# Kernel tuning notes

Measured on AMD Instinct MI355X. Metric: run time of the kernel, lower is better.

Reference implementation:

```python
import jax, jax.numpy as jnp
import numpy as np

B, C, H, W = 4, 128, 128, 128
G, K = 4, 3
P = K * K
STRIDE, PAD, DIL = 1, 1, 1
OFFSET_SCALE = 1.0


def setup_inputs() -> dict:
    key = jax.random.key(0)
    k1, k2, k3, k4 = jax.random.split(key, 4)
    inp = jax.random.normal(k1, (B, C, H, W), jnp.float32)
    # offset / mask linear params (zero-init in source; small random here for a
    # nontrivial sampling pattern -- same math, different param values)
    W_off = jax.random.normal(k2, (C, G * P * 2), jnp.float32) * 0.01
    b_off = jax.random.normal(k3, (G * P * 2,), jnp.float32) * 0.5
    W_mask = jax.random.normal(k4, (C, G * P), jnp.float32) * 0.02
    b_mask = jnp.zeros((G * P,), jnp.float32)
    return {"inp": inp, "W_off": W_off, "b_off": b_off, "W_mask": W_mask, "b_mask": b_mask}


def _dcnv3_core(x, offset, mask):
    # x: (b,h,w,c)  offset: (b,h,w,G*P*2)  mask: (b,h,w,G*P)
    b, h, w, c = x.shape
    gc = c // G
    xp = jnp.pad(x, ((0, 0), (PAD, PAD), (PAD, PAD), (0, 0)))
    H_in, W_in = h + 2 * PAD, w + 2 * PAD
    H_out = (H_in - (DIL * (K - 1) + 1)) // STRIDE + 1
    W_out = (W_in - (DIL * (K - 1) + 1)) // STRIDE + 1
    Q = H_out * W_out

    # reference points, normalized to padded size (matches _get_reference_points)
    base = (DIL * (K - 1)) // 2 + 0.5
    ref_y = (base + jnp.arange(H_out, dtype=jnp.float32) * STRIDE) / H_in
    ref_x = (base + jnp.arange(W_out, dtype=jnp.float32) * STRIDE) / W_in
    ref = jnp.stack(jnp.broadcast_arrays(ref_x[None, :], ref_y[:, None]), -1)  # (Ho,Wo,2) as (x,y)

    # dilation grid (matches _generate_dilation_grids; torch meshgrid flatten is x-major)
    off0 = -((DIL * (K - 1)) // 2)
    ks = off0 + jnp.arange(K, dtype=jnp.float32) * DIL
    gx = jnp.repeat(ks, K) / W_in  # (P,)
    gy = jnp.tile(ks, K) / H_in
    grid = jnp.stack([gx, gy], -1)  # (P,2), identical for every group

    norm = jnp.array([W_in, H_in], jnp.float32)
    loc = (ref[None, :, :, None, None, :]
           + grid[None, None, None, None, :, :] * OFFSET_SCALE
           + offset.reshape(b, H_out, W_out, G, P, 2) * (OFFSET_SCALE / norm))  # (b,Ho,Wo,G,P,2)

    # grid_sample(bilinear, zeros, align_corners=False): pixel = loc*size - 0.5
    px = loc[..., 0] * W_in - 0.5
    py = loc[..., 1] * H_in - 0.5
    x0 = jnp.floor(px); y0 = jnp.floor(py)
    tx = px - x0; ty = py - y0
    x0i = x0.astype(jnp.int32); y0i = y0.astype(jnp.int32)

    xg = xp.reshape(b, H_in * W_in, G, gc)

    def corner(ix, iy, wgt):
        valid = (ix >= 0) & (ix < W_in) & (iy >= 0) & (iy < H_in)
        lin = jnp.clip(iy, 0, H_in - 1) * W_in + jnp.clip(ix, 0, W_in - 1)
        idx = lin.reshape(b, Q, G, P).transpose(0, 1, 3, 2).reshape(b, Q * P, G)
        g = jnp.take_along_axis(xg, idx[..., None], axis=1)  # (b,Q*P,G,gc)
        wv = jnp.where(valid, wgt, 0.0).reshape(b, Q, G, P).transpose(0, 1, 3, 2).reshape(b, Q * P, G, 1)
        return g * wv

    val = (corner(x0i, y0i, (1 - tx) * (1 - ty))
           + corner(x0i + 1, y0i, tx * (1 - ty))
           + corner(x0i, y0i + 1, (1 - tx) * ty)
           + corner(x0i + 1, y0i + 1, tx * ty))  # (b,Q*P,G,gc)

    m = mask.reshape(b, Q, G, P).transpose(0, 1, 3, 2).reshape(b, Q, P, G, 1)
    out = (val.reshape(b, Q, P, G, gc) * m).sum(axis=2)  # (b,Q,G,gc)
    return out.reshape(b, H_out, W_out, G * gc)


def reference(inp, W_off, b_off, W_mask, b_mask):
    b, c, h, w = inp.shape
    x = inp.reshape(b, h, w, c)  # torch .view reinterpretation (faithful to source)
    offset = x @ W_off + b_off  # (b,h,w,G*P*2)
    mask = jax.nn.softmax((x @ W_mask + b_mask).reshape(b, h, w, G, P), axis=-1).reshape(b, h, w, G * P)
    out = _dcnv3_core(x, offset, mask)  # (b,h,w,c)
    return out.reshape(b, c, h, w)
```

## Files before the change

kernel.cpp:

```cpp
#include <hip/hip_runtime.h>


#define NPIX 65536

typedef unsigned int uint;
typedef unsigned short ushort;
typedef __attribute__((ext_vector_type(8))) short short8v;
typedef __attribute__((ext_vector_type(4))) float f32x4;

__device__ __forceinline__ ushort f2bf(float f) {
  uint u = __float_as_uint(f);
  u += 0x7FFFu + ((u >> 16) & 1u);
  return (ushort)(u >> 16);
}
__device__ __forceinline__ uint pkbf(float lo, float hi) {
  return (uint)f2bf(lo) | ((uint)f2bf(hi) << 16);
}
__device__ __forceinline__ float bflo(uint d) { return __uint_as_float(d << 16); }
__device__ __forceinline__ float bfhi(uint d) { return __uint_as_float(d & 0xFFFF0000u); }
__device__ __forceinline__ ushort f2h(float f) {
  union { _Float16 h; ushort u; } cv;
  cv.h = (_Float16)f;
  return cv.u;
}
__device__ __forceinline__ float h2f_lo(uint u) {
  union { ushort s; _Float16 h; } cv;
  cv.s = (ushort)(u & 0xFFFFu);
  return (float)cv.h;
}
__device__ __forceinline__ float h2f_hi(uint u) {
  union { ushort s; _Float16 h; } cv;
  cv.s = (ushort)(u >> 16);
  return (float)cv.h;
}

union U8 { uint u[4]; short8v v; };

__device__ __forceinline__ float wcol(const float* __restrict__ Woff,
                                      const float* __restrict__ Wmask,
                                      int g, int k, int n) {
  if (n < 18) return Woff[k * 72 + g * 18 + n];
  if (n < 27) return Wmask[k * 36 + g * 9 + (n - 18)];
  return 0.f;
}

__global__ __launch_bounds__(256) void dcn_wpack(
    const float* __restrict__ Woff, const float* __restrict__ boff,
    const float* __restrict__ Wmask, const float* __restrict__ bmask,
    uint* __restrict__ wpk, float* __restrict__ wb) {
  const int idx = (blockIdx.x << 8) + threadIdx.x;
  {
    const int f = idx >> 8;
    const int widx = idx & 255;
    const int lane = widx >> 2, epair = widx & 3;
    const int kt = f & 3, nt = (f >> 2) & 1, g = f >> 3;
    const int k0 = kt * 32 + (lane >> 4) * 8 + epair * 2;
    const int n = nt * 16 + (lane & 15);
    wpk[idx] = pkbf(wcol(Woff, Wmask, g, k0, n), wcol(Woff, Wmask, g, k0 + 1, n));
  }
  if (blockIdx.x == 0 && threadIdx.x < 128) {
    const int g = threadIdx.x >> 5, n = threadIdx.x & 31;
    float bv;
    if (n < 18) bv = boff[g * 18 + n];
    else if (n < 27) bv = bmask[g * 9 + (n - 18)];
    else bv = 0.f;
    wb[threadIdx.x] = bv;
  }
}

__global__ __launch_bounds__(256) void dcn_lin2(
    const float* __restrict__ x, const uint* __restrict__ wpk,
    const float* __restrict__ wb, ushort* __restrict__ ws16,
    ushort* __restrict__ x16) {
  __shared__ __align__(16) uint lds[64 * 68];
  const int pbase = blockIdx.x << 6;
  const int t = threadIdx.x;

  {
    const int px = t >> 2, part = t & 3;
    const int pix = pbase + px;
    const float* xp = x + (size_t)pix * 128 + part * 8;
    const int bb = pix >> 14, yx = pix & 16383;
#pragma unroll
    for (int g = 0; g < 4; ++g) {
      const float4 a = *(const float4*)(xp + g * 32);
      const float4 b4 = *(const float4*)(xp + g * 32 + 4);
      uint4 s;
      s.x = pkbf(a.x, a.y);
      s.y = pkbf(a.z, a.w);
      s.z = pkbf(b4.x, b4.y);
      s.w = pkbf(b4.z, b4.w);
      *(uint4*)(lds + px * 68 + g * 16 + part * 4) = s;
      *(uint4*)(x16 + ((((size_t)((g << 2) | bb) << 14) | yx) << 5) + part * 8) = s;
    }
  }
  __syncthreads();

  const int wv = t >> 6;
  const int lane = t & 63;
  const int lrow = lane & 15;
  const int lhi = lane >> 4;
  const int pxrow = (wv << 4) + lrow;

  U8 afr[4];
#pragma unroll
  for (int kt = 0; kt < 4; ++kt) {
    const uint4 v = *(const uint4*)(lds + pxrow * 68 + kt * 16 + lhi * 4);
    afr[kt].u[0] = v.x; afr[kt].u[1] = v.y;
    afr[kt].u[2] = v.z; afr[kt].u[3] = v.w;
  }
  __syncthreads();

  f32x4 acc[4][2];
#pragma unroll
  for (int g = 0; g < 4; ++g)
#pragma unroll
    for (int nt = 0; nt < 2; ++nt) {
      const float bv = wb[(g << 5) + (nt << 4) + lrow];
      acc[g][nt] = (f32x4){bv, bv, bv, bv};
    }

#pragma unroll
  for (int kt = 0; kt < 4; ++kt)
#pragma unroll
    for (int g = 0; g < 4; ++g)
#pragma unroll
      for (int nt = 0; nt < 2; ++nt) {
        U8 bf;
        const uint4 bv =
            *(const uint4*)(wpk + ((g << 3) + (nt << 2) + kt) * 256 + (lane << 2));
        bf.u[0] = bv.x; bf.u[1] = bv.y; bf.u[2] = bv.z; bf.u[3] = bv.w;
        acc[g][nt] =
            __builtin_amdgcn_mfma_f32_16x16x32_bf16(afr[kt].v, bf.v, acc[g][nt], 0, 0, 0);
      }

  {
    ushort* rec = (ushort*)lds;
    const int px0 = (wv << 4) + (lhi << 2);
#pragma unroll
    for (int g = 0; g < 4; ++g)
#pragma unroll
      for (int nt = 0; nt < 2; ++nt)
#pragma unroll
        for (int j = 0; j < 4; ++j)
          rec[(px0 + j) * 136 + (g << 5) + (nt << 4) + lrow] = f2h(acc[g][nt][j]);
  }
  __syncthreads();

  {
    const ushort* rec = (const ushort*)lds;
    ushort* dst = ws16 + (size_t)pbase * 128;
#pragma unroll
    for (int i = 0; i < 4; ++i) {
      const int idx = (i << 8) + t;
      const int px = idx >> 4;
      const int col = (idx & 15) << 3;
      const uint4 v = *(const uint4*)(rec + px * 136 + col);
      *(uint4*)(dst + (size_t)idx * 8) = v;
    }
  }
}

__global__ __launch_bounds__(256) void dcn_samp(
    const ushort* __restrict__ x16, const ushort* __restrict__ ws16,
    float* __restrict__ out) {
  const int g = blockIdx.x & 3;
  const int pg = threadIdx.x >> 2;
  const int sub = threadIdx.x & 3;
  const int q = ((blockIdx.x >> 2) << 6) | pg;
  const int b = q >> 14;
  const int h = (q >> 7) & 127;
  const int w = q & 127;
  const ushort* xg = x16 + (((size_t)((g << 2) | b)) << 19) + (sub << 3);

  const ushort* wsrec = ws16 + (size_t)q * 128 + (g << 5);
  const uint4 r0 = *(const uint4*)(wsrec);
  const uint4 r1 = *(const uint4*)(wsrec + 8);
  const uint4 r2 = *(const uint4*)(wsrec + 16);
  const uint2 r3 = *(const uint2*)(wsrec + 24);
  const uint rr0 = r0.x, rr1 = r0.y, rr2 = r0.z, rr3 = r0.w;
  const uint rr4 = r1.x, rr5 = r1.y, rr6 = r1.z, rr7 = r1.w;
  const uint rr8 = r2.x, rr9 = r2.y, rr10 = r2.z, rr11 = r2.w;
  const uint rr12 = r3.x, rr13 = r3.y;

  float offx9[9], offy9[9], mk9[9];
  {
    const uint rra[14] = {rr0, rr1, rr2,  rr3,  rr4,  rr5,  rr6,
                          rr7, rr8, rr9, rr10, rr11, rr12, rr13};
#pragma unroll
    for (int p = 0; p < 9; ++p) {
      offx9[p] = h2f_lo(rra[p]);
      offy9[p] = h2f_hi(rra[p]);
      const int li = 18 + p;
      mk9[p] = (li & 1) ? h2f_hi(rra[li >> 1]) : h2f_lo(rra[li >> 1]);
    }
    float mx = mk9[0];
#pragma unroll
    for (int p = 1; p < 9; ++p) mx = fmaxf(mx, mk9[p]);
    float s = 0.f;
#pragma unroll
    for (int p = 0; p < 9; ++p) {
      mk9[p] = __expf(mk9[p] - mx);
      s += mk9[p];
    }
    const float sinv = 1.0f / s;
#pragma unroll
    for (int p = 0; p < 9; ++p) mk9[p] *= sinv;
  }

  float a0 = 0.f, a1 = 0.f, a2 = 0.f, a3 = 0.f;
  float a4 = 0.f, a5 = 0.f, a6 = 0.f, a7 = 0.f;

#pragma unroll
  for (int p = 0; p < 9; ++p) {
    const float mk = mk9[p];
    const float px = (float)(w + p / 3) + offx9[p];
    const float py = (float)(h + p % 3) + offy9[p];
    const float fx = floorf(px), fy = floorf(py);
    const float tx = px - fx, ty = py - fy;
    const int x0 = (int)fx - 1, y0 = (int)fy - 1;
    const int x1 = x0 + 1, y1 = y0 + 1;
    const float ax0 = ((unsigned)x0 < 128u) ? (1.f - tx) : 0.f;
    const float ax1 = ((unsigned)x1 < 128u) ? tx : 0.f;
    const float ay0 = ((unsigned)y0 < 128u) ? (mk * (1.f - ty)) : 0.f;
    const float ay1 = ((unsigned)y1 < 128u) ? (mk * ty) : 0.f;
    const float w00 = ax0 * ay0, w10 = ax1 * ay0;
    const float w01 = ax0 * ay1, w11 = ax1 * ay1;
    const int cx0 = min(max(x0, 0), 127), cy0 = min(max(y0, 0), 127);
    const int cx1 = min(max(x1, 0), 127), cy1 = min(max(y1, 0), 127);
    const int o00 = ((cy0 << 7) | cx0) << 5;
    const int o10 = ((cy0 << 7) | cx1) << 5;
    const int o01 = ((cy1 << 7) | cx0) << 5;
    const int o11 = ((cy1 << 7) | cx1) << 5;
    const uint4 d00 = *(const uint4*)(xg + o00);
    const uint4 d10 = *(const uint4*)(xg + o10);
    const uint4 d01 = *(const uint4*)(xg + o01);
    const uint4 d11 = *(const uint4*)(xg + o11);
    a0 = fmaf(w00, bflo(d00.x), fmaf(w10, bflo(d10.x),
         fmaf(w01, bflo(d01.x), fmaf(w11, bflo(d11.x), a0))));
    a1 = fmaf(w00, bfhi(d00.x), fmaf(w10, bfhi(d10.x),
         fmaf(w01, bfhi(d01.x), fmaf(w11, bfhi(d11.x), a1))));
    a2 = fmaf(w00, bflo(d00.y), fmaf(w10, bflo(d10.y),
         fmaf(w01, bflo(d01.y), fmaf(w11, bflo(d11.y), a2))));
    a3 = fmaf(w00, bfhi(d00.y), fmaf(w10, bfhi(d10.y),
         fmaf(w01, bfhi(d01.y), fmaf(w11, bfhi(d11.y), a3))));
    a4 = fmaf(w00, bflo(d00.z), fmaf(w10, bflo(d10.z),
         fmaf(w01, bflo(d01.z), fmaf(w11, bflo(d11.z), a4))));
    a5 = fmaf(w00, bfhi(d00.z), fmaf(w10, bfhi(d10.z),
         fmaf(w01, bfhi(d01.z), fmaf(w11, bfhi(d11.z), a5))));
    a6 = fmaf(w00, bflo(d00.w), fmaf(w10, bflo(d10.w),
         fmaf(w01, bflo(d01.w), fmaf(w11, bflo(d11.w), a6))));
    a7 = fmaf(w00, bfhi(d00.w), fmaf(w10, bfhi(d10.w),
         fmaf(w01, bfhi(d01.w), fmaf(w11, bfhi(d11.w), a7))));
  }

  float* op = out + (size_t)q * 128 + (g << 5) + (sub << 3);
  float4 oa, ob;
  oa.x = a0; oa.y = a1; oa.z = a2; oa.w = a3;
  ob.x = a4; ob.y = a5; ob.z = a6; ob.w = a7;
  *(float4*)op = oa;
  *(float4*)(op + 4) = ob;
}

__global__ __launch_bounds__(256) void dcn_lin(
    const float* __restrict__ x, const float* __restrict__ Woff,
    const float* __restrict__ boff, const float* __restrict__ Wmask,
    const float* __restrict__ bmask, float* __restrict__ ws) {
  const int jg = blockIdx.x >> 8;
  const int pix = ((blockIdx.x & 255) << 8) | threadIdx.x;
  const float* W;
  const float* bias;
  int ldw, obase;
  if (jg == 0) {
    W = Woff; bias = boff; ldw = 72; obase = 0;
  } else if (jg == 1) {
    W = Woff + 36; bias = boff + 36; ldw = 72; obase = 36;
  } else {
    W = Wmask; bias = bmask; ldw = 36; obase = 72;
  }
  float acc[36];
#pragma unroll
  for (int j = 0; j < 36; ++j) acc[j] = bias[j];
  const float* xp = x + (size_t)pix * 128;
  for (int c0 = 0; c0 < 128; c0 += 8) {
    float xr[8];
    *(float4*)(xr) = *(const float4*)(xp + c0);
    *(float4*)(xr + 4) = *(const float4*)(xp + c0 + 4);
#pragma unroll
    for (int cc = 0; cc < 8; ++cc) {
      const float xc = xr[cc];
      const float* wr = W + (size_t)(c0 + cc) * ldw;
#pragma unroll
      for (int j = 0; j < 36; ++j) acc[j] = fmaf(xc, wr[j], acc[j]);
    }
  }
  if (jg == 2) {
#pragma unroll
    for (int g = 0; g < 4; ++g) {
      float mx = acc[g * 9];
#pragma unroll
      for (int p = 1; p < 9; ++p) mx = fmaxf(mx, acc[g * 9 + p]);
      float s = 0.f;
#pragma unroll
      for (int p = 0; p < 9; ++p) {
        acc[g * 9 + p] = __expf(acc[g * 9 + p] - mx);
        s += acc[g * 9 + p];
      }
      const float sinv = 1.0f / s;
#pragma unroll
      for (int p = 0; p < 9; ++p) acc[g * 9 + p] *= sinv;
    }
  }
#pragma unroll
  for (int j = 0; j < 36; ++j) ws[(size_t)(obase + j) * NPIX + pix] = acc[j];
}

__global__ __launch_bounds__(256) void dcn_samp_f32(
    const float* __restrict__ x, const float* __restrict__ ws,
    float* __restrict__ out) {
  const int q = (blockIdx.x << 4) | (threadIdx.x >> 4);
  const int sub = threadIdx.x & 15;
  const int c = sub << 3;
  const int g = sub >> 2;
  const int b = q >> 14;
  const int h = (q >> 7) & 127;
  const int w = q & 127;
  const float* xb = x + ((size_t)b << 21) + c;
  const float* wsq = ws + q;
  float a0 = 0.f, a1 = 0.f, a2 = 0.f, a3 = 0.f;
  float a4 = 0.f, a5 = 0.f, a6 = 0.f, a7 = 0.f;
#pragma unroll
  for (int p = 0; p < 9; ++p) {
    const float offx = wsq[(size_t)(g * 18 + p * 2) * NPIX];
    const float offy = wsq[(size_t)(g * 18 + p * 2 + 1) * NPIX];
    const float mk = wsq[(size_t)(72 + g * 9 + p) * NPIX];
    const float px = (float)(w + p / 3) + offx;
    const float py = (float)(h + p % 3) + offy;
    const float fx = floorf(px), fy = floorf(py);
    const float tx = px - fx, ty = py - fy;
    const int x0 = (int)fx - 1, y0 = (int)fy - 1;
    const int x1 = x0 + 1, y1 = y0 + 1;
    const float ax0 = ((unsigned)x0 < 128u) ? (1.f - tx) : 0.f;
    const float ax1 = ((unsigned)x1 < 128u) ? tx : 0.f;
    const float ay0 = ((unsigned)y0 < 128u) ? (mk * (1.f - ty)) : 0.f;
    const float ay1 = ((unsigned)y1 < 128u) ? (mk * ty) : 0.f;
    const float w00 = ax0 * ay0, w10 = ax1 * ay0;
    const float w01 = ax0 * ay1, w11 = ax1 * ay1;
    const int cx0 = min(max(x0, 0), 127), cy0 = min(max(y0, 0), 127);
    const int cx1 = min(max(x1, 0), 127), cy1 = min(max(y1, 0), 127);
    const int o00 = (cy0 << 14) | (cx0 << 7), o10 = (cy0 << 14) | (cx1 << 7);
    const int o01 = (cy1 << 14) | (cx0 << 7), o11 = (cy1 << 14) | (cx1 << 7);
    const float4 v00a = *(const float4*)(xb + o00);
    const float4 v00b = *(const float4*)(xb + o00 + 4);
    const float4 v10a = *(const float4*)(xb + o10);
    const float4 v10b = *(const float4*)(xb + o10 + 4);
    const float4 v01a = *(const float4*)(xb + o01);
    const float4 v01b = *(const float4*)(xb + o01 + 4);
    const float4 v11a = *(const float4*)(xb + o11);
    const float4 v11b = *(const float4*)(xb + o11 + 4);
    a0 = fmaf(w00, v00a.x, fmaf(w10, v10a.x, fmaf(w01, v01a.x, fmaf(w11, v11a.x, a0))));
    a1 = fmaf(w00, v00a.y, fmaf(w10, v10a.y, fmaf(w01, v01a.y, fmaf(w11, v11a.y, a1))));
    a2 = fmaf(w00, v00a.z, fmaf(w10, v10a.z, fmaf(w01, v01a.z, fmaf(w11, v11a.z, a2))));
    a3 = fmaf(w00, v00a.w, fmaf(w10, v10a.w, fmaf(w01, v01a.w, fmaf(w11, v11a.w, a3))));
    a4 = fmaf(w00, v00b.x, fmaf(w10, v10b.x, fmaf(w01, v01b.x, fmaf(w11, v11b.x, a4))));
    a5 = fmaf(w00, v00b.y, fmaf(w10, v10b.y, fmaf(w01, v01b.y, fmaf(w11, v11b.y, a5))));
    a6 = fmaf(w00, v00b.z, fmaf(w10, v10b.z, fmaf(w01, v01b.z, fmaf(w11, v11b.z, a6))));
    a7 = fmaf(w00, v00b.w, fmaf(w10, v10b.w, fmaf(w01, v01b.w, fmaf(w11, v11b.w, a7))));
  }
  float4 oa, ob;
  oa.x = a0; oa.y = a1; oa.z = a2; oa.w = a3;
  ob.x = a4; ob.y = a5; ob.z = a6; ob.w = a7;
  float* op = out + (size_t)q * 128 + c;
  *(float4*)op = oa;
  *(float4*)(op + 4) = ob;
}

__global__ __launch_bounds__(128) void dcn_fused(
    const float* __restrict__ x, const float* __restrict__ Woff,
    const float* __restrict__ boff, const float* __restrict__ Wmask,
    const float* __restrict__ bmask, float* __restrict__ out) {
  __shared__ float xs[128];
  __shared__ float res[108];
  __shared__ float msk[36];
  const int q = blockIdx.x;
  const int t = threadIdx.x;
  const int b = q >> 14, h = (q >> 7) & 127, w = q & 127;
  xs[t] = x[(size_t)q * 128 + t];
  __syncthreads();
  if (t < 108) {
    float a;
    const float* W;
    int ld;
    if (t < 72) {
      a = boff[t]; W = Woff + t; ld = 72;
    } else {
      a = bmask[t - 72]; W = Wmask + (t - 72); ld = 36;
    }
    for (int cc = 0; cc < 128; ++cc) a = fmaf(xs[cc], W[(size_t)cc * ld], a);
    res[t] = a;
  }
  __syncthreads();
  if (t < 4) {
    float mx = -1e30f;
    for (int p = 0; p < 9; ++p) mx = fmaxf(mx, res[72 + t * 9 + p]);
    float s = 0.f;
    float e[9];
    for (int p = 0; p < 9; ++p) {
      e[p] = __expf(res[72 + t * 9 + p] - mx);
      s += e[p];
    }
    for (int p = 0; p < 9; ++p) msk[t * 9 + p] = e[p] / s;
  }
  __syncthreads();
  const int g = t >> 5;
  const float* xb = x + ((size_t)b << 21) + t;
  float acc = 0.f;
#pragma unroll
  for (int p = 0; p < 9; ++p) {
    const float offx = res[g * 18 + p * 2];
    const float offy = res[g * 18 + p * 2 + 1];
    const float px = (float)(w + p / 3) + offx;
    const float py = (float)(h + p % 3) + offy;
    const float fx = floorf(px), fy = floorf(py);
    const float tx = px - fx, ty = py - fy;
    const int x0 = (int)fx - 1, y0 = (int)fy - 1;
    float sv = 0.f;
#define CORNER1(XI, YI, WT)                                       \
  if ((unsigned)(XI) < 128u && (unsigned)(YI) < 128u)             \
    sv = fmaf((WT), xb[((size_t)(YI) << 14) + ((size_t)(XI) << 7)], sv);
    CORNER1(x0, y0, (1.f - tx) * (1.f - ty))
    CORNER1(x0 + 1, y0, tx * (1.f - ty))
    CORNER1(x0, y0 + 1, (1.f - tx) * ty)
    CORNER1(x0 + 1, y0 + 1, tx * ty)
#undef CORNER1
    acc = fmaf(msk[g * 9 + p], sv, acc);
  }
  out[(size_t)q * 128 + t] = acc;
}

extern "C" void kernel_launch(void* const* d_in, const int* in_sizes, int n_in,
                              void* d_out, int out_size, void* d_ws,
                              size_t ws_size, hipStream_t stream) {
  const float* x = (const float*)d_in[0];
  const float* Woff = (const float*)d_in[1];
  const float* boff = (const float*)d_in[2];
  const float* Wmask = (const float*)d_in[3];
  const float* bmask = (const float*)d_in[4];
  float* out = (float*)d_out;
  const size_t x16_bytes = (size_t)NPIX * 128 * sizeof(ushort);
  const size_t ws16_bytes = (size_t)NPIX * 128 * sizeof(ushort);
  const size_t wpk_bytes = 8192 * sizeof(uint);
  const size_t need_full = x16_bytes + ws16_bytes + wpk_bytes + 512;
  const size_t need_ws = (size_t)NPIX * 108 * sizeof(float);
  if (ws_size >= need_full) {
    ushort* x16 = (ushort*)d_ws;
    ushort* ws16 = (ushort*)((char*)d_ws + x16_bytes);
    uint* wpk = (uint*)((char*)d_ws + x16_bytes + ws16_bytes);
    float* wb = (float*)((char*)d_ws + x16_bytes + ws16_bytes + wpk_bytes);
    dcn_wpack<<<32, 256, 0, stream>>>(Woff, boff, Wmask, bmask, wpk, wb);
    dcn_lin2<<<1024, 256, 0, stream>>>(x, wpk, wb, ws16, x16);
    dcn_samp<<<4096, 256, 0, stream>>>(x16, ws16, out);
  } else if (ws_size >= need_ws) {
    float* ws = (float*)d_ws;
    dcn_lin<<<768, 256, 0, stream>>>(x, Woff, boff, Wmask, bmask, ws);
    dcn_samp_f32<<<4096, 256, 0, stream>>>(x, ws, out);
  } else {
    dcn_fused<<<NPIX, 128, 0, stream>>>(x, Woff, boff, Wmask, bmask, out);
  }
}
```

Measured before the change: 53.62 us.

## Split bf16 pack from MFMA linear into separate kernels with single-wave blocks

The fused linear kernel, which both packed x to bf16 and ran the offset/mask MFMA projection, becomes two kernels. A pack kernel writes x16, then a 64-thread single-wave linear kernel reads its A fragments straight from x16 in global memory instead of LDS. This removes the block-wide barriers and the large LDS staging and allows many more small blocks. The cost is an extra kernel launch and a re-read of x16 from global memory or L2.

```diff
diff --git a/kernel.cpp b/kernel.cpp
--- a/kernel.cpp
+++ b/kernel.cpp
@@ -68,48 +68,45 @@
   }
 }
 
-__global__ __launch_bounds__(256) void dcn_lin2(
-    const float* __restrict__ x, const uint* __restrict__ wpk,
-    const float* __restrict__ wb, ushort* __restrict__ ws16,
-    ushort* __restrict__ x16) {
-  __shared__ __align__(16) uint lds[64 * 68];
-  const int pbase = blockIdx.x << 6;
+__global__ __launch_bounds__(128) void dcn_pack(
+    const float* __restrict__ x, ushort* __restrict__ x16) {
   const int t = threadIdx.x;
-
-  {
-    const int px = t >> 2, part = t & 3;
-    const int pix = pbase + px;
-    const float* xp = x + (size_t)pix * 128 + part * 8;
-    const int bb = pix >> 14, yx = pix & 16383;
-#pragma unroll
-    for (int g = 0; g < 4; ++g) {
-      const float4 a = *(const float4*)(xp + g * 32);
-      const float4 b4 = *(const float4*)(xp + g * 32 + 4);
-      uint4 s;
-      s.x = pkbf(a.x, a.y);
-      s.y = pkbf(a.z, a.w);
-      s.z = pkbf(b4.x, b4.y);
-      s.w = pkbf(b4.z, b4.w);
-      *(uint4*)(lds + px * 68 + g * 16 + part * 4) = s;
-      *(uint4*)(x16 + ((((size_t)((g << 2) | bb) << 14) | yx) << 5) + part * 8) = s;
-    }
-  }
-  __syncthreads();
-
-  const int wv = t >> 6;
-  const int lane = t & 63;
+  const int pix = (blockIdx.x << 5) + (t >> 2);
+  const int part = t & 3;
+  const float* xp = x + (size_t)pix * 128 + part * 8;
+  const int bb = pix >> 14, yx = pix & 16383;
+#pragma unroll
+  for (int g = 0; g < 4; ++g) {
+    const float4 a = *(const float4*)(xp + g * 32);
+    const float4 b4 = *(const float4*)(xp + g * 32 + 4);
+    uint4 s;
+    s.x = pkbf(a.x, a.y);
+    s.y = pkbf(a.z, a.w);
+    s.z = pkbf(b4.x, b4.y);
+    s.w = pkbf(b4.z, b4.w);
+    *(uint4*)(x16 + ((((size_t)((g << 2) | bb) << 14) | yx) << 5) + part * 8) = s;
+  }
+}
+
+__global__ __launch_bounds__(64) void dcn_lin3(
+    const ushort* __restrict__ x16, const uint* __restrict__ wpk,
+    const float* __restrict__ wb, ushort* __restrict__ ws16) {
+  __shared__ __align__(16) ushort rec[16 * 136];
+  const int pbase = blockIdx.x << 4;
+  const int lane = threadIdx.x;
   const int lrow = lane & 15;
   const int lhi = lane >> 4;
-  const int pxrow = (wv << 4) + lrow;
+  const int b = pbase >> 14;
+  const int yx = (pbase + lrow) & 16383;
 
   U8 afr[4];
 #pragma unroll
   for (int kt = 0; kt < 4; ++kt) {
-    const uint4 v = *(const uint4*)(lds + pxrow * 68 + kt * 16 + lhi * 4);
+    const uint4 v = *(const uint4*)(
+        x16 + ((((size_t)((kt << 2) | b) << 14) | yx) << 5) + (lhi << 3));
     afr[kt].u[0] = v.x; afr[kt].u[1] = v.y;
     afr[kt].u[2] = v.z; afr[kt].u[3] = v.w;
   }
-  __syncthreads();
 
   f32x4 acc[4][2];
 #pragma unroll
@@ -135,8 +132,7 @@
       }
 
   {
-    ushort* rec = (ushort*)lds;
-    const int px0 = (wv << 4) + (lhi << 2);
+    const int px0 = lhi << 2;
 #pragma unroll
     for (int g = 0; g < 4; ++g)
 #pragma unroll
@@ -148,15 +144,14 @@
   __syncthreads();
 
   {
-    const ushort* rec = (const ushort*)lds;
     ushort* dst = ws16 + (size_t)pbase * 128;
 #pragma unroll
     for (int i = 0; i < 4; ++i) {
-      const int idx = (i << 8) + t;
-      const int px = idx >> 4;
-      const int col = (idx & 15) << 3;
-      const uint4 v = *(const uint4*)(rec + px * 136 + col);
-      *(uint4*)(dst + (size_t)idx * 8) = v;
+      const int chunk = (i << 6) + lane;
+      const int px = chunk >> 4;
+      const int c8 = (chunk & 15) << 3;
+      const uint4 v = *(const uint4*)(rec + px * 136 + c8);
+      *(uint4*)(dst + (size_t)chunk * 8) = v;
     }
   }
 }
@@ -458,7 +453,8 @@
     uint* wpk = (uint*)((char*)d_ws + x16_bytes + ws16_bytes);
     float* wb = (float*)((char*)d_ws + x16_bytes + ws16_bytes + wpk_bytes);
     dcn_wpack<<<32, 256, 0, stream>>>(Woff, boff, Wmask, bmask, wpk, wb);
-    dcn_lin2<<<1024, 256, 0, stream>>>(x, wpk, wb, ws16, x16);
+    dcn_pack<<<2048, 128, 0, stream>>>(x, x16);
+    dcn_lin3<<<4096, 64, 0, stream>>>(x16, wpk, wb, ws16);
     dcn_samp<<<4096, 256, 0, stream>>>(x16, ws16, out);
   } else if (ws_size >= need_ws) {
     float* ws = (float*)d_ws;
```

New measurement: 58.83 us. 1.1x slower.
